# Performance work log

Measured on AMD Instinct MI355X. Metric: run time of the kernel, lower is better.

## Reference

```python
import jax, jax.numpy as jnp
import numpy as np

N_NODES = 50000
N_EDGES = 800000
BATCH = 128
D_IN = 768
D_H = 256
EPS_BN = 1e-5
EPS_COS = 1e-8


def setup_inputs() -> dict:
    key = jax.random.key(0)
    ks = jax.random.split(key, 16)
    s = 0.05
    return {
        "claim_embeddings": jax.random.normal(ks[0], (BATCH, D_IN), jnp.float32),
        "x": jax.random.normal(ks[1], (N_NODES, D_IN), jnp.float32),
        "edge_index": jax.random.randint(ks[2], (2, N_EDGES), 0, N_NODES, jnp.int32),
        "batch": jnp.sort(jax.random.randint(ks[3], (N_NODES,), 0, BATCH, jnp.int32)),
        "W1": jax.random.normal(ks[4], (D_IN, D_H), jnp.float32) * s,
        "a_src1": jax.random.normal(ks[5], (D_H,), jnp.float32) * s,
        "a_dst1": jax.random.normal(ks[6], (D_H,), jnp.float32) * s,
        "b1": jnp.zeros((D_H,), jnp.float32),
        "W2": jax.random.normal(ks[7], (D_H, D_H), jnp.float32) * s,
        "a_src2": jax.random.normal(ks[8], (D_H,), jnp.float32) * s,
        "a_dst2": jax.random.normal(ks[9], (D_H,), jnp.float32) * s,
        "b2": jnp.zeros((D_H,), jnp.float32),
        "bn_gamma": jnp.ones((D_H,), jnp.float32),
        "bn_beta": jnp.zeros((D_H,), jnp.float32),
        "Wc": jax.random.normal(ks[10], (D_H + D_IN, 1), jnp.float32) * s,
        "bc": jnp.zeros((1,), jnp.float32),
    }


def _gat_layer(h_in, src, dst, W, a_s, a_d, b, n_nodes):
    """PyG GATConv (heads=1, concat=True, self-loops already in src/dst)."""
    h = h_in @ W                                   # [N, D_H]
    alpha_s = h @ a_s                               # [N]
    alpha_d = h @ a_d                               # [N]
    e = jax.nn.leaky_relu(alpha_s[src] + alpha_d[dst], 0.2)  # [E+N]
    # numerically-stable softmax segmented by destination node
    e = e - jax.ops.segment_max(e, dst, num_segments=n_nodes)[dst]
    w = jnp.exp(e)
    w = w / jax.ops.segment_sum(w, dst, num_segments=n_nodes)[dst]
    out = jax.ops.segment_sum(h[src] * w[:, None], dst, num_segments=n_nodes)
    return out + b


def reference(claim_embeddings, x, edge_index, batch,
              W1, a_src1, a_dst1, b1, W2, a_src2, a_dst2, b2,
              bn_gamma, bn_beta, Wc, bc):
    n = x.shape[0]
    n_graphs = claim_embeddings.shape[0]
    # cosine-similarity relevance gating (torch eps semantics)
    ce = claim_embeddings[batch]                    # [N, D_IN]
    denom = jnp.maximum(jnp.linalg.norm(ce, axis=-1) * jnp.linalg.norm(x, axis=-1), EPS_COS)
    rel = jnp.sum(ce * x, axis=-1) / denom          # [N]
    h = x * rel[:, None]
    # add self-loops once (GATConv default add_self_loops=True)
    loops = jnp.arange(n, dtype=edge_index.dtype)
    src = jnp.concatenate([edge_index[0], loops])
    dst = jnp.concatenate([edge_index[1], loops])
    # layer 1 + batchnorm (batch stats) + relu
    h = _gat_layer(h, src, dst, W1, a_src1, a_dst1, b1, n)
    mean = jnp.mean(h, axis=0)
    var = jnp.mean(jnp.square(h - mean), axis=0)
    h = bn_gamma * (h - mean) * jax.lax.rsqrt(var + EPS_BN) + bn_beta
    h = jax.nn.relu(h)
    # layer 2 + relu
    h = _gat_layer(h, src, dst, W2, a_src2, a_dst2, b2, n)
    h = jax.nn.relu(h)
    # global mean pool per graph
    sums = jax.ops.segment_sum(h, batch, num_segments=n_graphs)
    counts = jax.ops.segment_sum(jnp.ones((n,), h.dtype), batch, num_segments=n_graphs)
    pooled = sums / jnp.maximum(counts, 1.0)[:, None]   # [B, D_H]
    combined = jnp.concatenate([pooled, claim_embeddings], axis=1)  # [B, D_H+D_IN]
    out = combined @ Wc + bc                        # [B, 1]
    return out.squeeze(-1)
```

## Files before the change

### kernel.cpp

```cpp
#include <hip/hip_runtime.h>
#include <hip/hip_bf16.h>

#define DIN 768
#define DH  256

typedef unsigned short ushort_t;
typedef __attribute__((ext_vector_type(8))) short short8v;
typedef __attribute__((ext_vector_type(4))) float f32x4;

__host__ __device__ inline int orig_col(int s) {
  return (s & ~63) | (s & 0x20) | ((s & 1) << 4) | ((s >> 1) & 0xF);
}

__device__ inline float wave_sum(float v) {
#pragma unroll
  for (int o = 32; o; o >>= 1) v += __shfl_xor(v, o);
  return v;
}
__device__ inline float leaky(float v) { return v > 0.f ? v : 0.2f * v; }

__device__ inline ushort_t f2bf(float f) {
  union { float f; unsigned u; } v; v.f = f;
  unsigned r = v.u + 0x7FFFu + ((v.u >> 16) & 1u);
  return (ushort_t)(r >> 16);
}
__device__ inline float bf2f(ushort_t u) {
  union { unsigned u; float f; } t; t.u = ((unsigned)u) << 16; return t.f;
}

__device__ inline void unpack8(uint4 v, float* f) {
  union { unsigned u; float f; } t;
  t.u = v.x << 16;         f[0] = t.f;
  t.u = v.x & 0xFFFF0000u; f[1] = t.f;
  t.u = v.y << 16;         f[2] = t.f;
  t.u = v.y & 0xFFFF0000u; f[3] = t.f;
  t.u = v.z << 16;         f[4] = t.f;
  t.u = v.z & 0xFFFF0000u; f[5] = t.f;
  t.u = v.w << 16;         f[6] = t.f;
  t.u = v.w & 0xFFFF0000u; f[7] = t.f;
}
__device__ inline uint4 pack8(const float* f) {
  uint4 o;
  o.x = (unsigned)f2bf(f[0]) | ((unsigned)f2bf(f[1]) << 16);
  o.y = (unsigned)f2bf(f[2]) | ((unsigned)f2bf(f[3]) << 16);
  o.z = (unsigned)f2bf(f[4]) | ((unsigned)f2bf(f[5]) << 16);
  o.w = (unsigned)f2bf(f[6]) | ((unsigned)f2bf(f[7]) << 16);
  return o;
}

__global__ __launch_bounds__(256) void relxb_hist_kernel(
    const float* __restrict__ ce, const float* __restrict__ x,
    const int* __restrict__ batch, ushort_t* __restrict__ xb, int n,
    const int* __restrict__ edst, int E, int* __restrict__ cnt) {
  int node = blockIdx.x * 4 + (threadIdx.x >> 6);
  int lane = threadIdx.x & 63;
  if (node < n) {
    int g = batch[node];
    const float4* xr = (const float4*)(x + (size_t)node * DIN);
    const float4* cr = (const float4*)(ce + (size_t)g * DIN);
    float4 av[3];
    float dxy = 0.f, dxx = 0.f, dcc = 0.f;
#pragma unroll
    for (int i = 0; i < 3; i++) {
      float4 a = xr[lane + 64 * i];
      float4 b = cr[lane + 64 * i];
      av[i] = a;
      dxy += a.x*b.x + a.y*b.y + a.z*b.z + a.w*b.w;
      dxx += a.x*a.x + a.y*a.y + a.z*a.z + a.w*a.w;
      dcc += b.x*b.x + b.y*b.y + b.z*b.z + b.w*b.w;
    }
    dxy = wave_sum(dxy);
    dxx = wave_sum(dxx);
    dcc = wave_sum(dcc);
    float denom = fmaxf(sqrtf(dxx) * sqrtf(dcc), 1e-8f);
    float rel = dxy / denom;
#pragma unroll
    for (int i = 0; i < 3; i++) {
      float4 a = av[i];
      ushort4 o = make_ushort4(f2bf(a.x * rel), f2bf(a.y * rel),
                               f2bf(a.z * rel), f2bf(a.w * rel));
      *(ushort4*)&xb[(size_t)node * DIN + (lane + 64 * i) * 4] = o;
    }
  }
  for (int e = blockIdx.x * blockDim.x + threadIdx.x; e < E;
       e += gridDim.x * blockDim.x)
    atomicAdd(&cnt[edst[e]], 1);
}

__global__ __launch_bounds__(256) void prep_kernel(
    const float* __restrict__ W1, const float* __restrict__ W2,
    const float* __restrict__ b1, const float* __restrict__ b2,
    const float* __restrict__ gamma, const float* __restrict__ beta,
    const float* __restrict__ Wc,
    ushort_t* __restrict__ Wt1, ushort_t* __restrict__ Wt2,
    float* __restrict__ pb1, float* __restrict__ pb2,
    float* __restrict__ pgamma, float* __restrict__ pbeta,
    float* __restrict__ pWc) {
  __shared__ float tile[64][65];
  int b = blockIdx.x;
  int t = threadIdx.x;
  int r4 = t >> 6;
  int c64 = t & 63;
  if (b < 48) {
    int k0 = (b % 12) * 64, c0 = (b / 12) * 64;
#pragma unroll
    for (int rr = 0; rr < 16; rr++) {
      int r = rr * 4 + r4;
      tile[r][c64] = W1[(size_t)(k0 + r) * 256 + c0 + c64];
    }
    __syncthreads();
#pragma unroll
    for (int rr = 0; rr < 16; rr++) {
      int cc = rr * 4 + r4;
      Wt1[(size_t)(c0 + cc) * DIN + k0 + c64] = f2bf(tile[c64][cc]);
    }
  } else if (b < 64) {
    int bb = b - 48;
    int k0 = (bb & 3) * 64, c0 = (bb >> 2) * 64;
#pragma unroll
    for (int rr = 0; rr < 16; rr++) {
      int r = rr * 4 + r4;
      tile[r][c64] = W2[(size_t)orig_col(k0 + r) * 256 + c0 + c64];
    }
    __syncthreads();
#pragma unroll
    for (int rr = 0; rr < 16; rr++) {
      int cc = rr * 4 + r4;
      Wt2[(size_t)(c0 + cc) * DH + k0 + c64] = f2bf(tile[c64][cc]);
    }
  } else {
    int o = orig_col(t);
    pb1[t] = b1[o];
    pb2[t] = b2[o];
    pgamma[t] = gamma[o];
    pbeta[t] = beta[o];
    pWc[t] = Wc[o];
  }
}

__global__ __launch_bounds__(1024) void scan_kernel(const int* __restrict__ cnt,
                                                    int* __restrict__ row_off, int n) {
  __shared__ int s[1024];
  int t = threadIdx.x;
  int chunk = (n + 1023) / 1024;
  int lo = t * chunk, hi = min(lo + chunk, n);
  int sum = 0;
  for (int i = lo; i < hi; i++) sum += cnt[i];
  int mysum = sum;
  s[t] = sum;
  __syncthreads();
  for (int off = 1; off < 1024; off <<= 1) {
    int v = (t >= off) ? s[t - off] : 0;
    __syncthreads();
    s[t] += v;
    __syncthreads();
  }
  int run = s[t] - mysum;
  for (int i = lo; i < hi; i++) { row_off[i] = run; run += cnt[i]; }
  if (t == 1023) row_off[n] = s[1023];
}

__global__ void fill_kernel(const int* __restrict__ src, const int* __restrict__ dst, int E,
                            const int* __restrict__ row_off, int* __restrict__ fill,
                            int* __restrict__ col_src) {
  for (int e = blockIdx.x * blockDim.x + threadIdx.x; e < E; e += gridDim.x * blockDim.x) {
    int d = dst[e];
    int slot = row_off[d] + atomicAdd(&fill[d], 1);
    col_src[slot] = src[e];
  }
}

template <int K>
__global__ __launch_bounds__(256) void gemm_mfma(
    const ushort_t* __restrict__ A, const ushort_t* __restrict__ Bt,
    ushort_t* __restrict__ C, const float* __restrict__ a_s,
    const float* __restrict__ a_d, float* __restrict__ alpha_s,
    float* __restrict__ alpha_d, int Mreal) {
  __shared__ ushort_t lds[16384];
  const int tid = threadIdx.x;
  const int lane = tid & 63;
  const int wave = tid >> 6;

  int p = blockIdx.y * 2 + blockIdx.x;
  int total = 2 * gridDim.y;
  int cch = p >> 4;
  int v;
  if ((cch << 4) + 16 <= total) {
    int r = p & 15;
    v = (cch << 4) | ((r & 7) << 1) | (r >> 3);
  } else {
    v = p;
  }
  const int col0 = (v & 1) * 128;
  const int row0 = (v >> 1) * 128;

  const int wr = wave >> 1, wc = wave & 1;
  const int c16 = lane & 15, g4 = lane >> 4;
  const int st_roff = lane >> 3;
  const int st_gsrc = (lane & 7) ^ st_roff;

  f32x4 acc[4][4];
#pragma unroll
  for (int m = 0; m < 4; m++)
#pragma unroll
    for (int nn = 0; nn < 4; nn++)
#pragma unroll
      for (int j = 0; j < 4; j++) acc[m][nn][j] = 0.f;

  for (int k0 = 0; k0 < K; k0 += 64) {
#pragma unroll
    for (int ci = 0; ci < 8; ci++) {
      int inst = wave * 8 + ci;
      int isB = inst >> 4;
      int idx = inst & 15;
      int lrow = idx * 8 + st_roff;
      const ushort_t* gsrc;
      if (isB == 0) {
        int rg = row0 + lrow;
        rg = rg < Mreal ? rg : Mreal - 1;
        gsrc = A + (size_t)rg * K + k0 + st_gsrc * 8;
      } else {
        gsrc = Bt + (size_t)(col0 + lrow) * K + k0 + st_gsrc * 8;
      }
      __builtin_amdgcn_global_load_lds(
          (const __attribute__((address_space(1))) void*)gsrc,
          (__attribute__((address_space(3))) void*)&lds[isB * 8192 + idx * 512],
          16, 0, 0);
    }
    __syncthreads();
#pragma unroll
    for (int ks = 0; ks < 2; ks++) {
      int g = ks * 4 + g4;
      short8v a[4], b[4];
#pragma unroll
      for (int m = 0; m < 4; m++) {
        int ra = wr * 64 + m * 16 + c16;
        a[m] = *(const short8v*)&lds[ra * 64 + (g ^ (ra & 7)) * 8];
      }
#pragma unroll
      for (int nn = 0; nn < 4; nn++) {
        int rb = wc * 64 + nn * 16 + c16;
        b[nn] = *(const short8v*)&lds[8192 + rb * 64 + (g ^ (rb & 7)) * 8];
      }
#pragma unroll
      for (int m = 0; m < 4; m++)
#pragma unroll
        for (int nn = 0; nn < 4; nn++)
          acc[m][nn] = __builtin_amdgcn_mfma_f32_16x16x32_bf16(a[m], b[nn],
                                                               acc[m][nn], 0, 0, 0);
    }
    __syncthreads();
  }

  float asv[4], adv[4];
#pragma unroll
  for (int nn = 0; nn < 4; nn++) {
    int col = col0 + wc * 64 + nn * 16 + c16;
    asv[nn] = a_s[col];
    adv[nn] = a_d[col];
  }

  uint* Cw = (uint*)C;
#pragma unroll
  for (int m = 0; m < 4; m++) {
    int row_base = row0 + wr * 64 + m * 16 + g4 * 4;
#pragma unroll
    for (int j = 0; j < 4; j++) {
      int row = row_base + j;
      float ps = 0.f, pd = 0.f;
#pragma unroll
      for (int nn = 0; nn < 4; nn++) {
        float v2 = acc[m][nn][j];
        ps = fmaf(v2, asv[nn], ps);
        pd = fmaf(v2, adv[nn], pd);
      }
#pragma unroll
      for (int o = 1; o < 16; o <<= 1) {
        ps += __shfl_xor(ps, o);
        pd += __shfl_xor(pd, o);
      }
      if (c16 == 0 && row < Mreal) {
        atomicAdd(&alpha_s[row], ps);
        atomicAdd(&alpha_d[row], pd);
      }
      if (row < Mreal) {
#pragma unroll
        for (int q = 0; q < 2; q++) {
          unsigned wv = (unsigned)f2bf(acc[m][2 * q][j]) |
                        ((unsigned)f2bf(acc[m][2 * q + 1][j]) << 16);
          Cw[(size_t)row * 128 + (col0 >> 1) + wc * 32 + q * 16 + c16] = wv;
        }
      }
    }
  }
}

__global__ __launch_bounds__(256) void gat_agg(
    const ushort_t* __restrict__ hb, const float* __restrict__ as_,
    const float* __restrict__ ad_, const int* __restrict__ row_off,
    const int* __restrict__ col_src, const float* __restrict__ bias,
    ushort_t* __restrict__ outb, int n, int relu_out) {
  int node = blockIdx.x * 4 + (threadIdx.x >> 6);
  int lane = threadIdx.x & 63;
  if (node >= n) return;
  int lo = row_off[node], hi = row_off[node + 1];
  int deg = hi - lo;
  float adn = ad_[node];
  float w_self = __expf(leaky(as_[node] + adn));

  const int q = lane >> 4;
  const int l16 = lane & 15;
  const ushort_t* rowbase = hb + (size_t)l16 * 16;

  float acc[16];
  float zacc = (lane == 0) ? w_self : 0.f;
  {
    const uint4* ps = (const uint4*)(rowbase + (size_t)node * 256);
    uint4 v0 = ps[0], v1 = ps[1];
    float ws = (q == 0) ? w_self : 0.f;
    float f[16];
    unpack8(v0, f);
    unpack8(v1, f + 8);
#pragma unroll
    for (int i = 0; i < 16; i++) acc[i] = ws * f[i];
  }

  for (int base = 0; base < deg; base += 64) {
    int cnt = min(64, deg - base);
    int s = 0; float w = 0.f;
    if (lane < cnt) {
      s = col_src[lo + base + lane];
      w = __expf(leaky(as_[s] + adn));
    }
    zacc += w;
    int e = 0;
    for (; e + 8 <= cnt; e += 8) {
      int iA = e + q, iB = e + 4 + q;
      int sA = __shfl(s, iA);
      float wA = __shfl(w, iA);
      int sB = __shfl(s, iB);
      float wB = __shfl(w, iB);
      const uint4* pA = (const uint4*)(rowbase + (size_t)sA * 256);
      const uint4* pB = (const uint4*)(rowbase + (size_t)sB * 256);
      uint4 a0 = pA[0], a1 = pA[1];
      uint4 b0 = pB[0], b1 = pB[1];
      float f[16];
      unpack8(a0, f);
      unpack8(a1, f + 8);
#pragma unroll
      for (int i = 0; i < 16; i++) acc[i] = fmaf(wA, f[i], acc[i]);
      unpack8(b0, f);
      unpack8(b1, f + 8);
#pragma unroll
      for (int i = 0; i < 16; i++) acc[i] = fmaf(wB, f[i], acc[i]);
    }
    for (; e < cnt; e += 4) {
      int myE = e + q;
      int idx = myE < cnt ? myE : cnt - 1;
      int ss = __shfl(s, idx);
      float wv = __shfl(w, idx);
      float wgt = (myE < cnt) ? wv : 0.f;
      const uint4* pp = (const uint4*)(rowbase + (size_t)ss * 256);
      uint4 v0 = pp[0], v1 = pp[1];
      float f[16];
      unpack8(v0, f);
      unpack8(v1, f + 8);
#pragma unroll
      for (int i = 0; i < 16; i++) acc[i] = fmaf(wgt, f[i], acc[i]);
    }
  }

  float z = wave_sum(zacc);
  float inv_z = 1.0f / z;

#pragma unroll
  for (int i = 0; i < 16; i++) {
    acc[i] += __shfl_xor(acc[i], 16);
    acc[i] += __shfl_xor(acc[i], 32);
  }

  if (q == 0) {
    float o[16];
#pragma unroll
    for (int i = 0; i < 16; i += 4) {
      float4 bb = *(const float4*)&bias[l16 * 16 + i];
      o[i]     = fmaf(acc[i],     inv_z, bb.x);
      o[i + 1] = fmaf(acc[i + 1], inv_z, bb.y);
      o[i + 2] = fmaf(acc[i + 2], inv_z, bb.z);
      o[i + 3] = fmaf(acc[i + 3], inv_z, bb.w);
    }
    if (relu_out) {
#pragma unroll
      for (int i = 0; i < 16; i++) o[i] = fmaxf(o[i], 0.f);
    }
    uint4* op = (uint4*)(outb + (size_t)node * 256 + l16 * 16);
    op[0] = pack8(o);
    op[1] = pack8(o + 8);
  }
}

__global__ __launch_bounds__(256) void bn_stats(const ushort_t* __restrict__ h, int n,
                                                float* __restrict__ bsum,
                                                float* __restrict__ bsq) {
  int c = threadIdx.x;
  int rows_per_block = (n + gridDim.x - 1) / gridDim.x;
  int r0 = blockIdx.x * rows_per_block;
  int r1 = min(r0 + rows_per_block, n);
  float sum = 0.f, sq = 0.f;
  for (int r = r0; r < r1; r++) {
    float v = bf2f(h[(size_t)r * 256 + c]);
    sum += v;
    sq = fmaf(v, v, sq);
  }
  atomicAdd(&bsum[c], sum);
  atomicAdd(&bsq[c], sq);
}

__global__ __launch_bounds__(256) void bn_apply(const ushort_t* __restrict__ h,
                                                const float* __restrict__ bsum,
                                                const float* __restrict__ bsq,
                                                const float* __restrict__ gamma,
                                                const float* __restrict__ beta,
                                                ushort_t* __restrict__ h2b, int n) {
  int total4 = n * 64;
  float inv_n = 1.0f / (float)n;
  for (int f = blockIdx.x * blockDim.x + threadIdx.x; f < total4;
       f += gridDim.x * blockDim.x) {
    int c4 = f & 63;
    uint2 hv = ((const uint2*)h)[f];
    float v0, v1, v2, v3;
    {
      union { unsigned u; float fl; } t;
      t.u = hv.x << 16;         v0 = t.fl;
      t.u = hv.x & 0xFFFF0000u; v1 = t.fl;
      t.u = hv.y << 16;         v2 = t.fl;
      t.u = hv.y & 0xFFFF0000u; v3 = t.fl;
    }
    float4 sm = ((const float4*)bsum)[c4];
    float4 sl = ((const float4*)bsq)[c4];
    float4 g = ((const float4*)gamma)[c4];
    float4 bb = ((const float4*)beta)[c4];
    float m, var;
    m = sm.x * inv_n; var = sl.x * inv_n - m * m;
    v0 = fmaxf(g.x * (v0 - m) * rsqrtf(var + 1e-5f) + bb.x, 0.f);
    m = sm.y * inv_n; var = sl.y * inv_n - m * m;
    v1 = fmaxf(g.y * (v1 - m) * rsqrtf(var + 1e-5f) + bb.y, 0.f);
    m = sm.z * inv_n; var = sl.z * inv_n - m * m;
    v2 = fmaxf(g.z * (v2 - m) * rsqrtf(var + 1e-5f) + bb.z, 0.f);
    m = sm.w * inv_n; var = sl.w * inv_n - m * m;
    v3 = fmaxf(g.w * (v3 - m) * rsqrtf(var + 1e-5f) + bb.w, 0.f);
    uint2 o;
    o.x = (unsigned)f2bf(v0) | ((unsigned)f2bf(v1) << 16);
    o.y = (unsigned)f2bf(v2) | ((unsigned)f2bf(v3) << 16);
    ((uint2*)h2b)[f] = o;
  }
}

__device__ inline int lower_bound_dev(const int* a, int n, int v) {
  int lo = 0, hi = n;
  while (lo < hi) {
    int mid = (lo + hi) >> 1;
    if (a[mid] < v) lo = mid + 1; else hi = mid;
  }
  return lo;
}

#define POOL_CHUNKS 16
__global__ __launch_bounds__(256) void pool_partial(const ushort_t* __restrict__ h,
                                                    const int* __restrict__ batch, int n,
                                                    float* __restrict__ psum) {
  int g = blockIdx.x / POOL_CHUNKS;
  int c = blockIdx.x % POOL_CHUNKS;
  int lo = lower_bound_dev(batch, n, g);
  int hi = lower_bound_dev(batch, n, g + 1);
  int len = hi - lo;
  int r0 = lo + (int)(((long long)len * c) / POOL_CHUNKS);
  int r1 = lo + (int)(((long long)len * (c + 1)) / POOL_CHUNKS);
  if (r1 <= r0) return;
  float sum = 0.f;
  for (int r = r0; r < r1; r++) sum += bf2f(h[(size_t)r * 256 + threadIdx.x]);
  atomicAdd(&psum[(size_t)g * 256 + threadIdx.x], sum);
}

__global__ __launch_bounds__(256) void final_kernel(const float* __restrict__ psum,
                                                    const int* __restrict__ batch, int n,
                                                    const float* __restrict__ ce,
                                                    const float* __restrict__ pWc,
                                                    const float* __restrict__ Wc,
                                                    const float* __restrict__ bc,
                                                    float* __restrict__ out, int B) {
  int g = blockIdx.x;
  int t = threadIdx.x;
  int lo = lower_bound_dev(batch, n, g);
  int hi = lower_bound_dev(batch, n, g + 1);
  float inv_cnt = 1.0f / fmaxf((float)(hi - lo), 1.0f);
  float p = 0.f;
  p = fmaf(psum[(size_t)g * 256 + t] * inv_cnt, pWc[t], p);
  p = fmaf(ce[(size_t)g * 768 + t],        Wc[256 + t], p);
  p = fmaf(ce[(size_t)g * 768 + 256 + t],  Wc[512 + t], p);
  p = fmaf(ce[(size_t)g * 768 + 512 + t],  Wc[768 + t], p);
  __shared__ float red[256];
  red[t] = p;
  __syncthreads();
  for (int s = 128; s; s >>= 1) {
    if (t < s) red[t] += red[t + s];
    __syncthreads();
  }
  if (t == 0) out[g] = red[0] + bc[0];
}

extern "C" void kernel_launch(void* const* d_in, const int* in_sizes, int n_in,
                              void* d_out, int out_size, void* d_ws, size_t ws_size,
                              hipStream_t stream) {
  const float* ce    = (const float*)d_in[0];
  const float* x     = (const float*)d_in[1];
  const int*   edge  = (const int*)d_in[2];
  const int*   batch = (const int*)d_in[3];
  const float* W1    = (const float*)d_in[4];
  const float* a_s1  = (const float*)d_in[5];
  const float* a_d1  = (const float*)d_in[6];
  const float* b1    = (const float*)d_in[7];
  const float* W2    = (const float*)d_in[8];
  const float* a_s2  = (const float*)d_in[9];
  const float* a_d2  = (const float*)d_in[10];
  const float* b2    = (const float*)d_in[11];
  const float* gamma = (const float*)d_in[12];
  const float* beta  = (const float*)d_in[13];
  const float* Wc    = (const float*)d_in[14];
  const float* bc    = (const float*)d_in[15];

  const int B = in_sizes[0] / DIN;
  const int n = in_sizes[1] / DIN;
  const int E = in_sizes[2] / 2;
  const int* esrc = edge;
  const int* edst = edge + E;

  char* w = (char*)d_ws;
  size_t off = 0;
  auto carve = [&](size_t bytes) -> void* {
    void* p = w + off;
    off = (off + bytes + 255) & ~(size_t)255;
    return p;
  };
  size_t hbytes = (size_t)n * DH * 2;
  char*  R1      = (char*)carve((size_t)n * DIN * 2);
  ushort_t* xb    = (ushort_t*)R1;
  ushort_t* h1b   = (ushort_t*)R1;
  ushort_t* h2b   = (ushort_t*)(R1 + hbytes);
  ushort_t* buf_ob = (ushort_t*)(R1 + 2 * hbytes);
  ushort_t* buf_hb = (ushort_t*)carve(hbytes);
  int*   row_off = (int*)carve((size_t)(n + 1) * 4);
  int*   col_src = (int*)carve((size_t)E * 4);
  ushort_t* Wt1  = (ushort_t*)carve((size_t)DIN * DH * 2);
  ushort_t* Wt2  = (ushort_t*)carve((size_t)DH * DH * 2);
  float* pb1     = (float*)carve(DH * 4);
  float* pb2     = (float*)carve(DH * 4);
  float* pgamma  = (float*)carve(DH * 4);
  float* pbeta   = (float*)carve(DH * 4);
  float* pWc     = (float*)carve(DH * 4);
  char* zero0 = (char*)carve((size_t)n * 4);
  int*   cnt     = (int*)zero0;
  int*   fill    = (int*)carve((size_t)n * 4);
  float* as1buf  = (float*)carve((size_t)n * 4);
  float* ad1buf  = (float*)carve((size_t)n * 4);
  float* as2buf  = (float*)carve((size_t)n * 4);
  float* ad2buf  = (float*)carve((size_t)n * 4);
  float* bn_sum  = (float*)carve(DH * 4);
  float* bn_sq   = (float*)carve(DH * 4);
  float* psum    = (float*)carve((size_t)B * DH * 4);
  size_t zero_bytes = (size_t)((char*)(psum + (size_t)B * DH) - zero0);

  hipMemsetAsync(zero0, 0, zero_bytes, stream);

  const int gN4 = (n + 3) / 4;
  const int Mb = (n + 127) / 128;

  prep_kernel<<<65, 256, 0, stream>>>(W1, W2, b1, b2, gamma, beta, Wc,
                                      Wt1, Wt2, pb1, pb2, pgamma, pbeta, pWc);
  relxb_hist_kernel<<<gN4, 256, 0, stream>>>(ce, x, batch, xb, n, edst, E, cnt);
  scan_kernel<<<1, 1024, 0, stream>>>(cnt, row_off, n);
  fill_kernel<<<1024, 256, 0, stream>>>(esrc, edst, E, row_off, fill, col_src);

  gemm_mfma<DIN><<<dim3(2, Mb), 256, 0, stream>>>(xb, Wt1, buf_hb, a_s1, a_d1,
                                                  as1buf, ad1buf, n);
  gat_agg<<<gN4, 256, 0, stream>>>(buf_hb, as1buf, ad1buf, row_off, col_src, pb1,
                                   h1b, n, 0);
  bn_stats<<<512, 256, 0, stream>>>(h1b, n, bn_sum, bn_sq);
  bn_apply<<<2048, 256, 0, stream>>>(h1b, bn_sum, bn_sq, pgamma, pbeta, h2b, n);

  gemm_mfma<DH><<<dim3(2, Mb), 256, 0, stream>>>(h2b, Wt2, buf_hb, a_s2, a_d2,
                                                 as2buf, ad2buf, n);
  gat_agg<<<gN4, 256, 0, stream>>>(buf_hb, as2buf, ad2buf, row_off, col_src, pb2,
                                   buf_ob, n, 1);

  pool_partial<<<B * POOL_CHUNKS, 256, 0, stream>>>(buf_ob, batch, n, psum);
  final_kernel<<<B, 256, 0, stream>>>(psum, batch, n, ce, pWc, Wc, bc,
                                      (float*)d_out, B);
}
```

Before: 444.2 us.

## Defer relevance scaling into GEMM epilogue, precompute claim norms, parallelize scan

The relevance scalar is no longer applied before the bf16 conversion of x. It is stored per node and applied to the first GEMM's output rows in the epilogue, since (rel*x)W = rel*(xW). This removes the wait on the wave reduction before storing xb and frees the registers that held the x row. Claim-embedding norms are computed once per graph in prep_kernel instead of per node. The single-block serial scan is replaced by a three-kernel block-parallel scan. In exchange there are two extra launches, and bf16 rounding now happens on unscaled x, which slightly changes numerics.

```diff
diff --git a/kernel.cpp b/kernel.cpp
--- a/kernel.cpp
+++ b/kernel.cpp
@@ -16,6 +16,13 @@
 #pragma unroll
   for (int o = 32; o; o >>= 1) v += __shfl_xor(v, o);
   return v;
+}
+__device__ inline void wave_sum2(float& a, float& b) {
+#pragma unroll
+  for (int o = 32; o; o >>= 1) {
+    a += __shfl_xor(a, o);
+    b += __shfl_xor(b, o);
+  }
 }
 __device__ inline float leaky(float v) { return v > 0.f ? v : 0.2f * v; }
 
@@ -50,7 +57,8 @@
 
 __global__ __launch_bounds__(256) void relxb_hist_kernel(
     const float* __restrict__ ce, const float* __restrict__ x,
-    const int* __restrict__ batch, ushort_t* __restrict__ xb, int n,
+    const int* __restrict__ batch, const float* __restrict__ cenorm,
+    ushort_t* __restrict__ xb, float* __restrict__ rel, int n,
     const int* __restrict__ edst, int E, int* __restrict__ cnt) {
   int node = blockIdx.x * 4 + (threadIdx.x >> 6);
   int lane = threadIdx.x & 63;
@@ -58,28 +66,20 @@
     int g = batch[node];
     const float4* xr = (const float4*)(x + (size_t)node * DIN);
     const float4* cr = (const float4*)(ce + (size_t)g * DIN);
-    float4 av[3];
-    float dxy = 0.f, dxx = 0.f, dcc = 0.f;
+    float dxy = 0.f, dxx = 0.f;
 #pragma unroll
     for (int i = 0; i < 3; i++) {
       float4 a = xr[lane + 64 * i];
       float4 b = cr[lane + 64 * i];
-      av[i] = a;
+      ushort4 o = make_ushort4(f2bf(a.x), f2bf(a.y), f2bf(a.z), f2bf(a.w));
+      *(ushort4*)&xb[(size_t)node * DIN + (lane + 64 * i) * 4] = o;
       dxy += a.x*b.x + a.y*b.y + a.z*b.z + a.w*b.w;
       dxx += a.x*a.x + a.y*a.y + a.z*a.z + a.w*a.w;
-      dcc += b.x*b.x + b.y*b.y + b.z*b.z + b.w*b.w;
-    }
-    dxy = wave_sum(dxy);
-    dxx = wave_sum(dxx);
-    dcc = wave_sum(dcc);
-    float denom = fmaxf(sqrtf(dxx) * sqrtf(dcc), 1e-8f);
-    float rel = dxy / denom;
-#pragma unroll
-    for (int i = 0; i < 3; i++) {
-      float4 a = av[i];
-      ushort4 o = make_ushort4(f2bf(a.x * rel), f2bf(a.y * rel),
-                               f2bf(a.z * rel), f2bf(a.w * rel));
-      *(ushort4*)&xb[(size_t)node * DIN + (lane + 64 * i) * 4] = o;
+    }
+    wave_sum2(dxy, dxx);
+    if (lane == 0) {
+      float denom = fmaxf(sqrtf(dxx) * cenorm[g], 1e-8f);
+      rel[node] = dxy / denom;
     }
   }
   for (int e = blockIdx.x * blockDim.x + threadIdx.x; e < E;
@@ -91,11 +91,11 @@
     const float* __restrict__ W1, const float* __restrict__ W2,
     const float* __restrict__ b1, const float* __restrict__ b2,
     const float* __restrict__ gamma, const float* __restrict__ beta,
-    const float* __restrict__ Wc,
+    const float* __restrict__ Wc, const float* __restrict__ ce,
     ushort_t* __restrict__ Wt1, ushort_t* __restrict__ Wt2,
     float* __restrict__ pb1, float* __restrict__ pb2,
     float* __restrict__ pgamma, float* __restrict__ pbeta,
-    float* __restrict__ pWc) {
+    float* __restrict__ pWc, float* __restrict__ cenorm, int B) {
   __shared__ float tile[64][65];
   int b = blockIdx.x;
   int t = threadIdx.x;
@@ -128,36 +128,70 @@
       int cc = rr * 4 + r4;
       Wt2[(size_t)(c0 + cc) * DH + k0 + c64] = f2bf(tile[c64][cc]);
     }
-  } else {
+  } else if (b == 64) {
     int o = orig_col(t);
     pb1[t] = b1[o];
     pb2[t] = b2[o];
     pgamma[t] = gamma[o];
     pbeta[t] = beta[o];
     pWc[t] = Wc[o];
-  }
-}
-
-__global__ __launch_bounds__(1024) void scan_kernel(const int* __restrict__ cnt,
+  } else {
+    int lane = t & 63;
+    for (int g = r4; g < B; g += 4) {
+      const float4* cr = (const float4*)(ce + (size_t)g * DIN);
+      float s = 0.f;
+#pragma unroll
+      for (int i = 0; i < 3; i++) {
+        float4 v = cr[lane + 64 * i];
+        s += v.x*v.x + v.y*v.y + v.z*v.z + v.w*v.w;
+      }
+      s = wave_sum(s);
+      if (lane == 0) cenorm[g] = sqrtf(s);
+    }
+  }
+}
+
+__global__ __launch_bounds__(256) void scan1_kernel(const int* __restrict__ cnt,
+                                                    int* __restrict__ row_off,
+                                                    int* __restrict__ bsum, int n) {
+  __shared__ int s[256];
+  int t = threadIdx.x;
+  int i = blockIdx.x * 256 + t;
+  int v = (i < n) ? cnt[i] : 0;
+  s[t] = v;
+  __syncthreads();
+  for (int off = 1; off < 256; off <<= 1) {
+    int tmp = (t >= off) ? s[t - off] : 0;
+    __syncthreads();
+    s[t] += tmp;
+    __syncthreads();
+  }
+  if (i < n) row_off[i] = s[t] - v;
+  if (t == 255) bsum[blockIdx.x] = s[255];
+}
+
+__global__ __launch_bounds__(256) void scan2_kernel(const int* __restrict__ bsum,
+                                                    int* __restrict__ boff, int nb,
                                                     int* __restrict__ row_off, int n) {
-  __shared__ int s[1024];
+  __shared__ int s[256];
   int t = threadIdx.x;
-  int chunk = (n + 1023) / 1024;
-  int lo = t * chunk, hi = min(lo + chunk, n);
-  int sum = 0;
-  for (int i = lo; i < hi; i++) sum += cnt[i];
-  int mysum = sum;
-  s[t] = sum;
+  int v = (t < nb) ? bsum[t] : 0;
+  s[t] = v;
   __syncthreads();
-  for (int off = 1; off < 1024; off <<= 1) {
-    int v = (t >= off) ? s[t - off] : 0;
-    __syncthreads();
-    s[t] += v;
-    __syncthreads();
-  }
-  int run = s[t] - mysum;
-  for (int i = lo; i < hi; i++) { row_off[i] = run; run += cnt[i]; }
-  if (t == 1023) row_off[n] = s[1023];
+  for (int off = 1; off < 256; off <<= 1) {
+    int tmp = (t >= off) ? s[t - off] : 0;
+    __syncthreads();
+    s[t] += tmp;
+    __syncthreads();
+  }
+  if (t < nb) boff[t] = s[t] - v;
+  if (t == nb - 1) row_off[n] = s[t];
+}
+
+__global__ __launch_bounds__(256) void scan3_kernel(int* __restrict__ row_off,
+                                                    const int* __restrict__ boff, int n) {
+  int i = blockIdx.x * 256 + threadIdx.x;
+  if (i < n) row_off[i] += boff[blockIdx.x];
 }
 
 __global__ void fill_kernel(const int* __restrict__ src, const int* __restrict__ dst, int E,
@@ -173,9 +207,9 @@
 template <int K>
 __global__ __launch_bounds__(256) void gemm_mfma(
     const ushort_t* __restrict__ A, const ushort_t* __restrict__ Bt,
-    ushort_t* __restrict__ C, const float* __restrict__ a_s,
-    const float* __restrict__ a_d, float* __restrict__ alpha_s,
-    float* __restrict__ alpha_d, int Mreal) {
+    ushort_t* __restrict__ C, const float* __restrict__ scale,
+    const float* __restrict__ a_s, const float* __restrict__ a_d,
+    float* __restrict__ alpha_s, float* __restrict__ alpha_d, int Mreal) {
   __shared__ ushort_t lds[16384];
   const int tid = threadIdx.x;
   const int lane = tid & 63;
@@ -267,10 +301,14 @@
 #pragma unroll
     for (int j = 0; j < 4; j++) {
       int row = row_base + j;
+      int rc = row < Mreal ? row : Mreal - 1;
+      float s = scale ? scale[rc] : 1.0f;
+      float vs[4];
       float ps = 0.f, pd = 0.f;
 #pragma unroll
       for (int nn = 0; nn < 4; nn++) {
-        float v2 = acc[m][nn][j];
+        float v2 = acc[m][nn][j] * s;
+        vs[nn] = v2;
         ps = fmaf(v2, asv[nn], ps);
         pd = fmaf(v2, adv[nn], pd);
       }
@@ -286,8 +324,8 @@
       if (row < Mreal) {
 #pragma unroll
         for (int q = 0; q < 2; q++) {
-          unsigned wv = (unsigned)f2bf(acc[m][2 * q][j]) |
-                        ((unsigned)f2bf(acc[m][2 * q + 1][j]) << 16);
+          unsigned wv = (unsigned)f2bf(vs[2 * q]) |
+                        ((unsigned)f2bf(vs[2 * q + 1]) << 16);
           Cw[(size_t)row * 128 + (col0 >> 1) + wc * 32 + q * 16 + c16] = wv;
         }
       }
@@ -558,6 +596,10 @@
   float* pgamma  = (float*)carve(DH * 4);
   float* pbeta   = (float*)carve(DH * 4);
   float* pWc     = (float*)carve(DH * 4);
+  float* cenorm  = (float*)carve((size_t)B * 4);
+  float* rel     = (float*)carve((size_t)n * 4);
+  int*   sc_bsum = (int*)carve(256 * 4);
+  int*   sc_boff = (int*)carve(256 * 4);
   char* zero0 = (char*)carve((size_t)n * 4);
   int*   cnt     = (int*)zero0;
   int*   fill    = (int*)carve((size_t)n * 4);
@@ -574,22 +616,27 @@
 
   const int gN4 = (n + 3) / 4;
   const int Mb = (n + 127) / 128;
-
-  prep_kernel<<<65, 256, 0, stream>>>(W1, W2, b1, b2, gamma, beta, Wc,
-                                      Wt1, Wt2, pb1, pb2, pgamma, pbeta, pWc);
-  relxb_hist_kernel<<<gN4, 256, 0, stream>>>(ce, x, batch, xb, n, edst, E, cnt);
-  scan_kernel<<<1, 1024, 0, stream>>>(cnt, row_off, n);
+  const int nb = (n + 255) / 256;
+
+  prep_kernel<<<66, 256, 0, stream>>>(W1, W2, b1, b2, gamma, beta, Wc, ce,
+                                      Wt1, Wt2, pb1, pb2, pgamma, pbeta, pWc,
+                                      cenorm, B);
+  relxb_hist_kernel<<<gN4, 256, 0, stream>>>(ce, x, batch, cenorm, xb, rel, n,
+                                             edst, E, cnt);
+  scan1_kernel<<<nb, 256, 0, stream>>>(cnt, row_off, sc_bsum, n);
+  scan2_kernel<<<1, 256, 0, stream>>>(sc_bsum, sc_boff, nb, row_off, n);
+  scan3_kernel<<<nb, 256, 0, stream>>>(row_off, sc_boff, n);
   fill_kernel<<<1024, 256, 0, stream>>>(esrc, edst, E, row_off, fill, col_src);
 
-  gemm_mfma<DIN><<<dim3(2, Mb), 256, 0, stream>>>(xb, Wt1, buf_hb, a_s1, a_d1,
-                                                  as1buf, ad1buf, n);
+  gemm_mfma<DIN><<<dim3(2, Mb), 256, 0, stream>>>(xb, Wt1, buf_hb, rel, a_s1,
+                                                  a_d1, as1buf, ad1buf, n);
   gat_agg<<<gN4, 256, 0, stream>>>(buf_hb, as1buf, ad1buf, row_off, col_src, pb1,
                                    h1b, n, 0);
   bn_stats<<<512, 256, 0, stream>>>(h1b, n, bn_sum, bn_sq);
   bn_apply<<<2048, 256, 0, stream>>>(h1b, bn_sum, bn_sq, pgamma, pbeta, h2b, n);
 
-  gemm_mfma<DH><<<dim3(2, Mb), 256, 0, stream>>>(h2b, Wt2, buf_hb, a_s2, a_d2,
-                                                 as2buf, ad2buf, n);
+  gemm_mfma<DH><<<dim3(2, Mb), 256, 0, stream>>>(h2b, Wt2, buf_hb, nullptr, a_s2,
+                                                 a_d2, as2buf, ad2buf, n);
   gat_agg<<<gN4, 256, 0, stream>>>(buf_hb, as2buf, ad2buf, row_off, col_src, pb2,
                                    buf_ob, n, 1);
 
```

After: 417.8 us. 1.06x faster.
